# Optimization experiments

Hardware: AMD Instinct MI355X
Metric: run time of the kernel (lower is better)

Reference implementation:

```python
import jax, jax.numpy as jnp
import numpy as np

N_NODES = 50000
N_EDGES = 800000
D_IN = 128
D_HID = 128
BN_EPS = 1e-5


def _sage_mean(h, src, dst, w_self, w_neigh, b):
    # DGL SAGEConv('mean'): out = h @ W_self + mean_{neighbors}(h_src) @ W_neigh + bias
    msg = h[src]                                               # [E, D] gather
    ssum = jax.ops.segment_sum(msg, dst, num_segments=N_NODES)  # [N, D]
    deg = jax.ops.segment_sum(jnp.ones((src.shape[0],), h.dtype), dst,
                              num_segments=N_NODES)            # [N]
    mean = ssum / jnp.maximum(deg, 1.0)[:, None]
    return h @ w_self + mean @ w_neigh + b


def _bn_relu(h, gamma, beta):
    # BatchNorm1d with batch statistics (training-mode math), then ReLU.
    m = jnp.mean(h, axis=0)
    v = jnp.mean(jnp.square(h - m), axis=0)  # biased variance, as torch uses for normalization
    hn = (h - m) * jax.lax.rsqrt(v + BN_EPS) * gamma + beta
    return jax.nn.relu(hn)


def setup_inputs() -> dict:
    key = jax.random.key(0)
    ks = jax.random.split(key, 16)
    x = jax.random.normal(ks[0], (N_NODES, D_IN), dtype=jnp.float32)
    src = jax.random.randint(ks[1], (N_EDGES,), 0, N_NODES, dtype=jnp.int32)
    dst = jax.random.randint(ks[2], (N_EDGES,), 0, N_NODES, dtype=jnp.int32)
    s0 = 1.0 / np.sqrt(D_IN)
    s1 = 1.0 / np.sqrt(D_HID)
    inp = {
        'x': x, 'src': src, 'dst': dst,
        'W_self0': jax.random.uniform(ks[3], (D_IN, D_HID), jnp.float32, -s0, s0),
        'W_neigh0': jax.random.uniform(ks[4], (D_IN, D_HID), jnp.float32, -s0, s0),
        'b0': jnp.zeros((D_HID,), jnp.float32),
        'W_self1': jax.random.uniform(ks[5], (D_HID, D_HID), jnp.float32, -s1, s1),
        'W_neigh1': jax.random.uniform(ks[6], (D_HID, D_HID), jnp.float32, -s1, s1),
        'b1': jnp.zeros((D_HID,), jnp.float32),
        'W_self2': jax.random.uniform(ks[7], (D_HID, D_HID), jnp.float32, -s1, s1),
        'W_neigh2': jax.random.uniform(ks[8], (D_HID, D_HID), jnp.float32, -s1, s1),
        'b2': jnp.zeros((D_HID,), jnp.float32),
        'gamma0': jnp.ones((D_HID,), jnp.float32),
        'beta0': jnp.zeros((D_HID,), jnp.float32),
        'gamma1': jnp.ones((D_HID,), jnp.float32),
        'beta1': jnp.zeros((D_HID,), jnp.float32),
    }
    return inp


def reference(x, src, dst,
              W_self0, W_neigh0, b0,
              W_self1, W_neigh1, b1,
              W_self2, W_neigh2, b2,
              gamma0, beta0, gamma1, beta1):
    h = _sage_mean(x, src, dst, W_self0, W_neigh0, b0)
    h = _bn_relu(h, gamma0, beta0)  # dropout is identity in eval mode
    h = _sage_mean(h, src, dst, W_self1, W_neigh1, b1)
    h = _bn_relu(h, gamma1, beta1)
    h = _sage_mean(h, src, dst, W_self2, W_neigh2, b2)
    return h
```

## Files before the change

kernel.cpp:

```cpp
#include <hip/hip_runtime.h>

#define N_NODES 50000
#define N_EDGES 800000
#define D 128
#define BN_EPS 1e-5f

#define NBUCK 391
#define BSHIFT 7
#define S1_BLOCKS 256
#define EPB 3125
#define CVT_BLOCKS 6250
#define PACK_BLOCKS 384
#define NREP 8

typedef __attribute__((ext_vector_type(8))) short bf16x8;
typedef __attribute__((ext_vector_type(4))) float f32x4;

__device__ inline unsigned short f2bf(float f) {
    unsigned int u = __float_as_uint(f);
    u = (u + 0x7FFF + ((u >> 16) & 1)) >> 16;
    return (unsigned short)u;
}

__device__ inline float bf2f(unsigned short b) {
    return __uint_as_float(((unsigned)b) << 16);
}

__device__ __forceinline__ void acc_plain(float* a, uint4 v) {
    unsigned w[4] = {v.x, v.y, v.z, v.w};
#pragma unroll
    for (int p = 0; p < 4; p++) {
        a[2 * p]     += __uint_as_float(w[p] << 16);
        a[2 * p + 1] += __uint_as_float(w[p] & 0xffff0000u);
    }
}

__device__ __forceinline__ void acc_bn(float* a, uint4 v, const float* sc, const float* sh) {
    unsigned w[4] = {v.x, v.y, v.z, v.w};
#pragma unroll
    for (int p = 0; p < 4; p++) {
        float lo = __uint_as_float(w[p] << 16);
        float hi = __uint_as_float(w[p] & 0xffff0000u);
        a[2 * p]     += fmaxf(lo * sc[2 * p]     + sh[2 * p],     0.f);
        a[2 * p + 1] += fmaxf(hi * sc[2 * p + 1] + sh[2 * p + 1], 0.f);
    }
}


__global__ void fused_prep(const float* __restrict__ x, unsigned short* __restrict__ x16,
                           const int* __restrict__ dst, int* __restrict__ hist,
                           const float* __restrict__ Ws0, const float* __restrict__ Wn0,
                           const float* __restrict__ Ws1, const float* __restrict__ Wn1,
                           const float* __restrict__ Ws2, const float* __restrict__ Wn2,
                           unsigned short* __restrict__ Wf, float* __restrict__ statsg) {
    __shared__ int lh[NBUCK];
    const int bid = blockIdx.x, t = threadIdx.x;

    if (bid < CVT_BLOCKS) {
        int idx = bid * 256 + t;
        float4 v = ((const float4*)x)[idx];
        ushort4 o;
        o.x = f2bf(v.x); o.y = f2bf(v.y); o.z = f2bf(v.z); o.w = f2bf(v.w);
        ((ushort4*)x16)[idx] = o;
    } else if (bid < CVT_BLOCKS + S1_BLOCKS) {
        int blk = bid - CVT_BLOCKS;
        for (int i = t; i < NBUCK; i += 256) lh[i] = 0;
        __syncthreads();
        int e0 = blk * EPB;
        for (int i = 0; i < 13; i++) {
            int k = t + i * 256;
            if (k < EPB) atomicAdd(&lh[dst[e0 + k] >> BSHIFT], 1);
        }
        __syncthreads();
        for (int i = t; i < NBUCK; i += 256) hist[blk * NBUCK + i] = lh[i];
    } else {
        if (bid == CVT_BLOCKS + S1_BLOCKS) {
            for (int i = t; i < 2 * NREP * 256; i += 256) statsg[i] = 0.f;
        }
        int idx = (bid - (CVT_BLOCKS + S1_BLOCKS)) * 256 + t;
        if (idx < 3 * 32768) {
            int layer = idx >> 15;
            int rem = idx & 32767;
            int kt = rem >> 12;
            int nt = (rem >> 9) & 7;
            int lane = (rem >> 3) & 63;
            int j = rem & 7;
            int k = kt * 32 + (lane >> 4) * 8 + j;
            int n = nt * 16 + (lane & 15);
            const float* Wsrc;
            if (layer == 0) Wsrc = (k < 128) ? Ws0 : Wn0;
            else if (layer == 1) Wsrc = (k < 128) ? Ws1 : Wn1;
            else Wsrc = (k < 128) ? Ws2 : Wn2;
            Wf[idx] = f2bf(Wsrc[(k & 127) * D + n]);
        }
    }
}


__global__ void s2a(int* __restrict__ hist, int* __restrict__ bucketTotal) {
    __shared__ int s[S1_BLOCKS];
    int b = blockIdx.x, t = threadIdx.x;
    int v = hist[t * NBUCK + b];
    s[t] = v;
    __syncthreads();
    for (int off = 1; off < S1_BLOCKS; off <<= 1) {
        int x = (t >= off) ? s[t - off] : 0;
        __syncthreads();
        s[t] += x;
        __syncthreads();
    }
    hist[t * NBUCK + b] = s[t] - v;
    if (t == S1_BLOCKS - 1) bucketTotal[b] = s[t];
}


__global__ void s3_scatter(const int* __restrict__ src, const int* __restrict__ dst,
                           const int* __restrict__ hist, const int* __restrict__ bucketTotal,
                           int* __restrict__ bucketStart, unsigned int* __restrict__ rec) {
    __shared__ int sc[512];
    __shared__ int base[NBUCK];
    int blk = blockIdx.x, t = threadIdx.x;
    int i1 = t + 256;
    int v0 = (t < NBUCK) ? bucketTotal[t] : 0;
    int v1 = (i1 < NBUCK) ? bucketTotal[i1] : 0;
    sc[t] = v0; sc[i1] = v1;
    __syncthreads();
    for (int off = 1; off < 512; off <<= 1) {
        int x0 = (t >= off) ? sc[t - off] : 0;
        int x1 = (i1 >= off) ? sc[i1 - off] : 0;
        __syncthreads();
        sc[t] += x0; sc[i1] += x1;
        __syncthreads();
    }
    if (t < NBUCK)  base[t]  = (sc[t] - v0)  + hist[blk * NBUCK + t];
    if (i1 < NBUCK) base[i1] = (sc[i1] - v1) + hist[blk * NBUCK + i1];
    if (blk == 0) {
        if (t < NBUCK)  bucketStart[t]  = sc[t] - v0;
        if (i1 < NBUCK) bucketStart[i1] = sc[i1] - v1;
        if (t == 0) bucketStart[NBUCK] = N_EDGES;
    }
    __syncthreads();
    int e0 = blk * EPB;
    for (int i = 0; i < 13; i++) {
        int k = t + i * 256;
        if (k < EPB) {
            int e = e0 + k;
            int d = dst[e];
            int p = atomicAdd(&base[d >> BSHIFT], 1);
            rec[p] = ((unsigned)(d & 127) << 16) | (unsigned)src[e];
        }
    }
}


__global__ void s4_build(const unsigned int* __restrict__ rec, const int* __restrict__ bucketStart,
                         unsigned short* __restrict__ csr, int* __restrict__ degi,
                         int* __restrict__ offsets, float* __restrict__ inv_deg) {
    __shared__ int lh[128];
    __shared__ int ls[128];
    __shared__ int lcur[128];
    int b = blockIdx.x, t = threadIdx.x;
    int start = bucketStart[b], end = bucketStart[b + 1];

    if (t < 128) lh[t] = 0;
    __syncthreads();
    for (int e = start + t; e < end; e += 256)
        atomicAdd(&lh[rec[e] >> 16], 1);
    __syncthreads();

    int v = 0;
    if (t < 128) { v = lh[t]; ls[t] = v; }
    __syncthreads();
    for (int off = 1; off < 128; off <<= 1) {
        int x = 0;
        if (t < 128 && t >= off) x = ls[t - off];
        __syncthreads();
        if (t < 128) ls[t] += x;
        __syncthreads();
    }

    int node0 = b << BSHIFT;
    if (t < 128) {
        int excl = ls[t] - v;
        lcur[t] = start + excl;
        int node = node0 + t;
        if (node < N_NODES) {
            degi[node] = v;
            offsets[node] = start + excl;
            inv_deg[node] = 1.0f / (float)max(v, 1);
        }
    }
    __syncthreads();
    for (int e = start + t; e < end; e += 256) {
        unsigned r = rec[e];
        int p = atomicAdd(&lcur[r >> 16], 1);
        csr[p] = (unsigned short)(r & 0xFFFFu);
    }
}


#define GATHER(k) (*(const uint4*)(h16 + (size_t)csr[beg + (k)] * D + c * 8))

__global__ void aggregate16(const unsigned short* __restrict__ h16,
                            const unsigned short* __restrict__ csr, const int* __restrict__ offsets,
                            const int* __restrict__ degi, const float* __restrict__ inv_deg,
                            unsigned short* __restrict__ mean16,
                            const float* __restrict__ statsIn,
                            const float* __restrict__ gammaIn, const float* __restrict__ betaIn,
                            float* __restrict__ scshG) {
    int t = threadIdx.x;
    if (statsIn && blockIdx.x == 0 && t < 128) {
        const float invN = 1.0f / (float)N_NODES;
        float s = 0.f, q = 0.f;
#pragma unroll
        for (int r = 0; r < NREP; r++) {
            s += statsIn[r * 256 + t];
            q += statsIn[r * 256 + 128 + t];
        }
        float m = s * invN;
        float var = q * invN - m * m;
        float scv = rsqrtf(var + BN_EPS) * gammaIn[t];
        scshG[t] = scv;
        scshG[128 + t] = betaIn[t] - m * scv;
    }

    int node = blockIdx.x * 16 + (t >> 4);
    if (node >= N_NODES) return;
    int c = t & 15;
    int beg = offsets[node], n = degi[node];
    float a[8];
#pragma unroll
    for (int j = 0; j < 8; j++) a[j] = 0.f;

    if (statsIn) {
        const float invN = 1.0f / (float)N_NODES;
        float sc[8], sh[8];
#pragma unroll
        for (int j = 0; j < 8; j++) {
            int col = c * 8 + j;
            float s = 0.f, q = 0.f;
#pragma unroll
            for (int r = 0; r < NREP; r++) {
                s += statsIn[r * 256 + col];
                q += statsIn[r * 256 + 128 + col];
            }
            float m = s * invN;
            float var = q * invN - m * m;
            float scv = rsqrtf(var + BN_EPS) * gammaIn[col];
            sc[j] = scv;
            sh[j] = betaIn[col] - m * scv;
        }
        int i = 0;
        if (n >= 4) {
            uint4 v0 = GATHER(0), v1 = GATHER(1), v2 = GATHER(2), v3 = GATHER(3);
            for (i = 4; i + 3 < n; i += 4) {
                uint4 w0 = GATHER(i), w1 = GATHER(i + 1), w2 = GATHER(i + 2), w3 = GATHER(i + 3);
                acc_bn(a, v0, sc, sh); acc_bn(a, v1, sc, sh);
                acc_bn(a, v2, sc, sh); acc_bn(a, v3, sc, sh);
                v0 = w0; v1 = w1; v2 = w2; v3 = w3;
            }
            acc_bn(a, v0, sc, sh); acc_bn(a, v1, sc, sh);
            acc_bn(a, v2, sc, sh); acc_bn(a, v3, sc, sh);
        }
        for (; i < n; i++) { uint4 v = GATHER(i); acc_bn(a, v, sc, sh); }
    } else {
        int i = 0;
        if (n >= 4) {
            uint4 v0 = GATHER(0), v1 = GATHER(1), v2 = GATHER(2), v3 = GATHER(3);
            for (i = 4; i + 3 < n; i += 4) {
                uint4 w0 = GATHER(i), w1 = GATHER(i + 1), w2 = GATHER(i + 2), w3 = GATHER(i + 3);
                acc_plain(a, v0); acc_plain(a, v1); acc_plain(a, v2); acc_plain(a, v3);
                v0 = w0; v1 = w1; v2 = w2; v3 = w3;
            }
            acc_plain(a, v0); acc_plain(a, v1); acc_plain(a, v2); acc_plain(a, v3);
        }
        for (; i < n; i++) { uint4 v = GATHER(i); acc_plain(a, v); }
    }

    float w = inv_deg[node];
    uint4 o;
    o.x = ((unsigned)f2bf(a[1] * w) << 16) | f2bf(a[0] * w);
    o.y = ((unsigned)f2bf(a[3] * w) << 16) | f2bf(a[2] * w);
    o.z = ((unsigned)f2bf(a[5] * w) << 16) | f2bf(a[4] * w);
    o.w = ((unsigned)f2bf(a[7] * w) << 16) | f2bf(a[6] * w);
    *(uint4*)(mean16 + (size_t)node * D + c * 8) = o;
}


__global__ __launch_bounds__(256, 4) void sage_gemm(
    const unsigned short* __restrict__ h16, const unsigned short* __restrict__ mean16,
    const unsigned short* __restrict__ Wf, const float* __restrict__ bias,
    unsigned short* __restrict__ out16, float* __restrict__ outf,
    float* __restrict__ statsOut, const float* __restrict__ scshG) {
    __shared__ unsigned short sWf[16384];
    __shared__ float sstat[256];
    const int t = threadIdx.x;
    const int lane = t & 63;
    const int m = lane & 15;
    const int quad = lane >> 4;
    const int wrow0 = blockIdx.x * 64 + (t >> 6) * 16;

    int arow = wrow0 + m;
    if (arow >= N_NODES) arow = N_NODES - 1;

    bf16x8 afr[8];
#pragma unroll
    for (int kt = 0; kt < 4; kt++)
        afr[kt] = *(const bf16x8*)(h16 + (size_t)arow * D + kt * 32 + quad * 8);
#pragma unroll
    for (int kt = 0; kt < 4; kt++)
        afr[4 + kt] = *(const bf16x8*)(mean16 + (size_t)arow * D + kt * 32 + quad * 8);

    const uint4* W4 = (const uint4*)Wf;
    uint4* S4 = (uint4*)sWf;
#pragma unroll
    for (int i = 0; i < 8; i++) S4[i * 256 + t] = W4[i * 256 + t];
    if (statsOut) sstat[t] = 0.f;
    __syncthreads();

    if (scshG) {
#pragma unroll
        for (int kt = 0; kt < 4; kt++) {
            int c0 = kt * 32 + quad * 8;
            float4 sca = *(const float4*)(scshG + c0);
            float4 scb = *(const float4*)(scshG + c0 + 4);
            float4 sha = *(const float4*)(scshG + 128 + c0);
            float4 shb = *(const float4*)(scshG + 128 + c0 + 4);
            float scv[8] = {sca.x, sca.y, sca.z, sca.w, scb.x, scb.y, scb.z, scb.w};
            float shv[8] = {sha.x, sha.y, sha.z, sha.w, shb.x, shb.y, shb.z, shb.w};
#pragma unroll
            for (int j = 0; j < 8; j++) {
                float v = fmaxf(bf2f((unsigned short)afr[kt][j]) * scv[j] + shv[j], 0.f);
                afr[kt][j] = (short)f2bf(v);
            }
        }
    }

    f32x4 acc[8];
#pragma unroll
    for (int i = 0; i < 8; i++) acc[i] = (f32x4)(0.f);

#pragma unroll
    for (int kt = 0; kt < 4; kt++) {
#pragma unroll
        for (int nt = 0; nt < 8; nt++) {
            bf16x8 bf = *(const bf16x8*)(sWf + ((kt * 8 + nt) * 64 + lane) * 8);
            acc[nt] = __builtin_amdgcn_mfma_f32_16x16x32_bf16(afr[kt], bf, acc[nt], 0, 0, 0);
        }
    }

    __syncthreads();
#pragma unroll
    for (int i = 0; i < 8; i++) S4[i * 256 + t] = W4[2048 + i * 256 + t];
    __syncthreads();

#pragma unroll
    for (int kt = 4; kt < 8; kt++) {
#pragma unroll
        for (int nt = 0; nt < 8; nt++) {
            bf16x8 bf = *(const bf16x8*)(sWf + (((kt - 4) * 8 + nt) * 64 + lane) * 8);
            acc[nt] = __builtin_amdgcn_mfma_f32_16x16x32_bf16(afr[kt], bf, acc[nt], 0, 0, 0);
        }
    }

    const bool do16 = (out16 != nullptr);
#pragma unroll
    for (int nt = 0; nt < 8; nt++) {
        int cidx = nt * 16 + m;
        float bv = bias[cidx];
        float s = 0.f, q = 0.f;
#pragma unroll
        for (int reg = 0; reg < 4; reg++) {
            int r = wrow0 + quad * 4 + reg;
            float v = acc[nt][reg] + bv;
            if (r < N_NODES) {
                if (do16) out16[(size_t)r * D + cidx] = f2bf(v);
                else      outf[(size_t)r * D + cidx] = v;
                s += v; q += v * v;
            }
        }
        if (statsOut) {
            s += __shfl_xor(s, 16); s += __shfl_xor(s, 32);
            q += __shfl_xor(q, 16); q += __shfl_xor(q, 32);
            if (quad == 0) {
                atomicAdd(&sstat[cidx], s);
                atomicAdd(&sstat[128 + cidx], q);
            }
        }
    }
    if (statsOut) {
        __syncthreads();
        atomicAdd(&statsOut[(blockIdx.x & (NREP - 1)) * 256 + t], sstat[t]);
    }
}


extern "C" void kernel_launch(void* const* d_in, const int* in_sizes, int n_in,
                              void* d_out, int out_size, void* d_ws, size_t ws_size,
                              hipStream_t stream) {
    const float* x   = (const float*)d_in[0];
    const int* src   = (const int*)d_in[1];
    const int* dst   = (const int*)d_in[2];
    const float* Ws0 = (const float*)d_in[3];
    const float* Wn0 = (const float*)d_in[4];
    const float* b0  = (const float*)d_in[5];
    const float* Ws1 = (const float*)d_in[6];
    const float* Wn1 = (const float*)d_in[7];
    const float* b1  = (const float*)d_in[8];
    const float* Ws2 = (const float*)d_in[9];
    const float* Wn2 = (const float*)d_in[10];
    const float* b2  = (const float*)d_in[11];
    const float* g0  = (const float*)d_in[12];
    const float* be0 = (const float*)d_in[13];
    const float* g1  = (const float*)d_in[14];
    const float* be1 = (const float*)d_in[15];

    char* base = (char*)d_ws;
    size_t NND = (size_t)N_NODES * D;
    unsigned short* X16    = (unsigned short*)base;
    unsigned short* H16    = (unsigned short*)(base + NND * 2);
    unsigned short* mean16 = (unsigned short*)(base + 2 * NND * 2);
    char* p = base + 6 * NND;
    unsigned short* Wf = (unsigned short*)p;  p += 3 * 32768 * 2;
    int* hist          = (int*)p;             p += (size_t)S1_BLOCKS * NBUCK * 4;
    int* bucketTotal   = (int*)p;             p += 1568;
    int* bucketStart   = (int*)p;             p += 1600;
    unsigned int* rec  = (unsigned int*)p;    p += (size_t)N_EDGES * 4;
    unsigned short* csr = (unsigned short*)p; p += (size_t)N_EDGES * 2;
    int* degi    = (int*)p;                   p += N_NODES * 4;
    int* offsets = (int*)p;                   p += N_NODES * 4;
    float* inv_deg = (float*)p;               p += N_NODES * 4;
    float* stats   = (float*)p;               p += 2 * NREP * 256 * 4;
    float* scsh    = (float*)p;               p += 1024;
    float* stats0 = stats, *stats1 = stats + NREP * 256;

    fused_prep<<<CVT_BLOCKS + S1_BLOCKS + PACK_BLOCKS, 256, 0, stream>>>(
        x, X16, dst, hist, Ws0, Wn0, Ws1, Wn1, Ws2, Wn2, Wf, stats);
    s2a<<<NBUCK, 256, 0, stream>>>(hist, bucketTotal);
    s3_scatter<<<S1_BLOCKS, 256, 0, stream>>>(src, dst, hist, bucketTotal, bucketStart, rec);
    s4_build<<<NBUCK, 256, 0, stream>>>(rec, bucketStart, csr, degi, offsets, inv_deg);

    const int AGG_B = (N_NODES + 15) / 16;
    const int GEMM_B = (N_NODES + 63) / 64;

    aggregate16<<<AGG_B, 256, 0, stream>>>(X16, csr, offsets, degi, inv_deg, mean16,
                                           nullptr, nullptr, nullptr, nullptr);
    sage_gemm<<<GEMM_B, 256, 0, stream>>>(X16, mean16, Wf, b0, H16, nullptr,
                                          stats0, nullptr);

    aggregate16<<<AGG_B, 256, 0, stream>>>(H16, csr, offsets, degi, inv_deg, mean16,
                                           stats0, g0, be0, scsh);
    sage_gemm<<<GEMM_B, 256, 0, stream>>>(H16, mean16, Wf + 32768, b1, X16, nullptr,
                                          stats1, scsh);

    aggregate16<<<AGG_B, 256, 0, stream>>>(X16, csr, offsets, degi, inv_deg, mean16,
                                           stats1, g1, be1, scsh);
    sage_gemm<<<GEMM_B, 256, 0, stream>>>(X16, mean16, Wf + 65536, b2, nullptr,
                                          (float*)d_out, nullptr, scsh);
}
```

Before: 311.2 us.

## Sort CSR neighbors by source slice and apply BN-ReLU in separate pass

The CSR build now buckets each node's neighbors by the high bits of the source index, so gathers within a node run in roughly ascending source order. This aims for better cache locality during aggregation. BatchNorm+ReLU is no longer applied per edge inside aggregation and again in the GEMM prologue; a standalone elementwise kernel normalizes the hidden activations in place once. The stats replica count is also doubled to reduce atomic contention. The separate BN pass adds an extra read and write of the activation tensor and two more launches.

```diff
diff --git a/kernel.cpp b/kernel.cpp
--- a/kernel.cpp
+++ b/kernel.cpp
@@ -11,7 +11,10 @@
 #define EPB 3125
 #define CVT_BLOCKS 6250
 #define PACK_BLOCKS 384
-#define NREP 8
+#define NREP 16
+#define NSLICE 8
+#define SSHIFT 13
+#define BN_BLOCKS 512
 
 typedef __attribute__((ext_vector_type(8))) short bf16x8;
 typedef __attribute__((ext_vector_type(4))) float f32x4;
@@ -32,17 +35,6 @@
     for (int p = 0; p < 4; p++) {
         a[2 * p]     += __uint_as_float(w[p] << 16);
         a[2 * p + 1] += __uint_as_float(w[p] & 0xffff0000u);
-    }
-}
-
-__device__ __forceinline__ void acc_bn(float* a, uint4 v, const float* sc, const float* sh) {
-    unsigned w[4] = {v.x, v.y, v.z, v.w};
-#pragma unroll
-    for (int p = 0; p < 4; p++) {
-        float lo = __uint_as_float(w[p] << 16);
-        float hi = __uint_as_float(w[p] & 0xffff0000u);
-        a[2 * p]     += fmaxf(lo * sc[2 * p]     + sh[2 * p],     0.f);
-        a[2 * p + 1] += fmaxf(hi * sc[2 * p + 1] + sh[2 * p + 1], 0.f);
     }
 }
 
@@ -156,45 +148,101 @@
 __global__ void s4_build(const unsigned int* __restrict__ rec, const int* __restrict__ bucketStart,
                          unsigned short* __restrict__ csr, int* __restrict__ degi,
                          int* __restrict__ offsets, float* __restrict__ inv_deg) {
-    __shared__ int lh[128];
-    __shared__ int ls[128];
-    __shared__ int lcur[128];
+    __shared__ int cnt[128 * NSLICE];
+    __shared__ int exc[128 * NSLICE];
+    __shared__ int lcur[128 * NSLICE];
+    __shared__ int ls[256];
     int b = blockIdx.x, t = threadIdx.x;
     int start = bucketStart[b], end = bucketStart[b + 1];
 
-    if (t < 128) lh[t] = 0;
-    __syncthreads();
-    for (int e = start + t; e < end; e += 256)
-        atomicAdd(&lh[rec[e] >> 16], 1);
-    __syncthreads();
-
-    int v = 0;
-    if (t < 128) { v = lh[t]; ls[t] = v; }
-    __syncthreads();
-    for (int off = 1; off < 128; off <<= 1) {
-        int x = 0;
-        if (t < 128 && t >= off) x = ls[t - off];
-        __syncthreads();
-        if (t < 128) ls[t] += x;
-        __syncthreads();
-    }
-
-    int node0 = b << BSHIFT;
+    for (int i = t; i < 128 * NSLICE; i += 256) cnt[i] = 0;
+    __syncthreads();
+    for (int e = start + t; e < end; e += 256) {
+        unsigned r = rec[e];
+        int key = ((r >> 16) << 3) | ((r & 0xFFFFu) >> SSHIFT);
+        atomicAdd(&cnt[key], 1);
+    }
+    __syncthreads();
+
+    int c0 = cnt[4 * t], c1 = cnt[4 * t + 1], c2 = cnt[4 * t + 2], c3 = cnt[4 * t + 3];
+    int sum4 = c0 + c1 + c2 + c3;
+    ls[t] = sum4;
+    __syncthreads();
+    for (int off = 1; off < 256; off <<= 1) {
+        int x = (t >= off) ? ls[t - off] : 0;
+        __syncthreads();
+        ls[t] += x;
+        __syncthreads();
+    }
+    int base = ls[t] - sum4;
+    exc[4 * t]     = base;
+    exc[4 * t + 1] = base + c0;
+    exc[4 * t + 2] = base + c0 + c1;
+    exc[4 * t + 3] = base + c0 + c1 + c2;
+    lcur[4 * t]     = start + base;
+    lcur[4 * t + 1] = start + base + c0;
+    lcur[4 * t + 2] = start + base + c0 + c1;
+    lcur[4 * t + 3] = start + base + c0 + c1 + c2;
+    __syncthreads();
+
     if (t < 128) {
-        int excl = ls[t] - v;
-        lcur[t] = start + excl;
-        int node = node0 + t;
+        int node = (b << BSHIFT) + t;
+        int e0 = exc[8 * t];
+        int e1 = (t == 127) ? (end - start) : exc[8 * t + 8];
+        int v = e1 - e0;
         if (node < N_NODES) {
             degi[node] = v;
-            offsets[node] = start + excl;
+            offsets[node] = start + e0;
             inv_deg[node] = 1.0f / (float)max(v, 1);
         }
     }
     __syncthreads();
     for (int e = start + t; e < end; e += 256) {
         unsigned r = rec[e];
-        int p = atomicAdd(&lcur[r >> 16], 1);
+        int key = ((r >> 16) << 3) | ((r & 0xFFFFu) >> SSHIFT);
+        int p = atomicAdd(&lcur[key], 1);
         csr[p] = (unsigned short)(r & 0xFFFFu);
+    }
+}
+
+
+__global__ void bn_relu_apply(unsigned short* __restrict__ h,
+                              const float* __restrict__ stats,
+                              const float* __restrict__ gamma, const float* __restrict__ beta) {
+    __shared__ float sc[128], sh[128];
+    int t = threadIdx.x;
+    if (t < 128) {
+        const float invN = 1.0f / (float)N_NODES;
+        float s = 0.f, q = 0.f;
+#pragma unroll
+        for (int r = 0; r < NREP; r++) {
+            s += stats[r * 256 + t];
+            q += stats[r * 256 + 128 + t];
+        }
+        float m = s * invN;
+        float var = q * invN - m * m;
+        float scv = rsqrtf(var + BN_EPS) * gamma[t];
+        sc[t] = scv;
+        sh[t] = beta[t] - m * scv;
+    }
+    __syncthreads();
+    const int total = N_NODES * D / 8;
+    for (int idx = blockIdx.x * 256 + t; idx < total; idx += BN_BLOCKS * 256) {
+        uint4 v = ((const uint4*)h)[idx];
+        int col0 = (idx & 15) * 8;
+        unsigned w[4] = {v.x, v.y, v.z, v.w};
+        unsigned ow[4];
+#pragma unroll
+        for (int p = 0; p < 4; p++) {
+            float lo = __uint_as_float(w[p] << 16);
+            float hi = __uint_as_float(w[p] & 0xffff0000u);
+            float rlo = fmaxf(lo * sc[col0 + 2 * p]     + sh[col0 + 2 * p],     0.f);
+            float rhi = fmaxf(hi * sc[col0 + 2 * p + 1] + sh[col0 + 2 * p + 1], 0.f);
+            ow[p] = ((unsigned)f2bf(rhi) << 16) | f2bf(rlo);
+        }
+        uint4 o;
+        o.x = ow[0]; o.y = ow[1]; o.z = ow[2]; o.w = ow[3];
+        ((uint4*)h)[idx] = o;
     }
 }
 
@@ -204,26 +252,8 @@
 __global__ void aggregate16(const unsigned short* __restrict__ h16,
                             const unsigned short* __restrict__ csr, const int* __restrict__ offsets,
                             const int* __restrict__ degi, const float* __restrict__ inv_deg,
-                            unsigned short* __restrict__ mean16,
-                            const float* __restrict__ statsIn,
-                            const float* __restrict__ gammaIn, const float* __restrict__ betaIn,
-                            float* __restrict__ scshG) {
+                            unsigned short* __restrict__ mean16) {
     int t = threadIdx.x;
-    if (statsIn && blockIdx.x == 0 && t < 128) {
-        const float invN = 1.0f / (float)N_NODES;
-        float s = 0.f, q = 0.f;
-#pragma unroll
-        for (int r = 0; r < NREP; r++) {
-            s += statsIn[r * 256 + t];
-            q += statsIn[r * 256 + 128 + t];
-        }
-        float m = s * invN;
-        float var = q * invN - m * m;
-        float scv = rsqrtf(var + BN_EPS) * gammaIn[t];
-        scshG[t] = scv;
-        scshG[128 + t] = betaIn[t] - m * scv;
-    }
-
     int node = blockIdx.x * 16 + (t >> 4);
     if (node >= N_NODES) return;
     int c = t & 15;
@@ -232,50 +262,17 @@
 #pragma unroll
     for (int j = 0; j < 8; j++) a[j] = 0.f;
 
-    if (statsIn) {
-        const float invN = 1.0f / (float)N_NODES;
-        float sc[8], sh[8];
-#pragma unroll
-        for (int j = 0; j < 8; j++) {
-            int col = c * 8 + j;
-            float s = 0.f, q = 0.f;
-#pragma unroll
-            for (int r = 0; r < NREP; r++) {
-                s += statsIn[r * 256 + col];
-                q += statsIn[r * 256 + 128 + col];
-            }
-            float m = s * invN;
-            float var = q * invN - m * m;
-            float scv = rsqrtf(var + BN_EPS) * gammaIn[col];
-            sc[j] = scv;
-            sh[j] = betaIn[col] - m * scv;
-        }
-        int i = 0;
-        if (n >= 4) {
-            uint4 v0 = GATHER(0), v1 = GATHER(1), v2 = GATHER(2), v3 = GATHER(3);
-            for (i = 4; i + 3 < n; i += 4) {
-                uint4 w0 = GATHER(i), w1 = GATHER(i + 1), w2 = GATHER(i + 2), w3 = GATHER(i + 3);
-                acc_bn(a, v0, sc, sh); acc_bn(a, v1, sc, sh);
-                acc_bn(a, v2, sc, sh); acc_bn(a, v3, sc, sh);
-                v0 = w0; v1 = w1; v2 = w2; v3 = w3;
-            }
-            acc_bn(a, v0, sc, sh); acc_bn(a, v1, sc, sh);
-            acc_bn(a, v2, sc, sh); acc_bn(a, v3, sc, sh);
-        }
-        for (; i < n; i++) { uint4 v = GATHER(i); acc_bn(a, v, sc, sh); }
-    } else {
-        int i = 0;
-        if (n >= 4) {
-            uint4 v0 = GATHER(0), v1 = GATHER(1), v2 = GATHER(2), v3 = GATHER(3);
-            for (i = 4; i + 3 < n; i += 4) {
-                uint4 w0 = GATHER(i), w1 = GATHER(i + 1), w2 = GATHER(i + 2), w3 = GATHER(i + 3);
-                acc_plain(a, v0); acc_plain(a, v1); acc_plain(a, v2); acc_plain(a, v3);
-                v0 = w0; v1 = w1; v2 = w2; v3 = w3;
-            }
+    int i = 0;
+    if (n >= 4) {
+        uint4 v0 = GATHER(0), v1 = GATHER(1), v2 = GATHER(2), v3 = GATHER(3);
+        for (i = 4; i + 3 < n; i += 4) {
+            uint4 w0 = GATHER(i), w1 = GATHER(i + 1), w2 = GATHER(i + 2), w3 = GATHER(i + 3);
             acc_plain(a, v0); acc_plain(a, v1); acc_plain(a, v2); acc_plain(a, v3);
-        }
-        for (; i < n; i++) { uint4 v = GATHER(i); acc_plain(a, v); }
-    }
+            v0 = w0; v1 = w1; v2 = w2; v3 = w3;
+        }
+        acc_plain(a, v0); acc_plain(a, v1); acc_plain(a, v2); acc_plain(a, v3);
+    }
+    for (; i < n; i++) { uint4 v = GATHER(i); acc_plain(a, v); }
 
     float w = inv_deg[node];
     uint4 o;
@@ -291,7 +288,7 @@
     const unsigned short* __restrict__ h16, const unsigned short* __restrict__ mean16,
     const unsigned short* __restrict__ Wf, const float* __restrict__ bias,
     unsigned short* __restrict__ out16, float* __restrict__ outf,
-    float* __restrict__ statsOut, const float* __restrict__ scshG) {
+    float* __restrict__ statsOut) {
     __shared__ unsigned short sWf[16384];
     __shared__ float sstat[256];
     const int t = threadIdx.x;
@@ -317,24 +314,6 @@
     for (int i = 0; i < 8; i++) S4[i * 256 + t] = W4[i * 256 + t];
     if (statsOut) sstat[t] = 0.f;
     __syncthreads();
-
-    if (scshG) {
-#pragma unroll
-        for (int kt = 0; kt < 4; kt++) {
-            int c0 = kt * 32 + quad * 8;
-            float4 sca = *(const float4*)(scshG + c0);
-            float4 scb = *(const float4*)(scshG + c0 + 4);
-            float4 sha = *(const float4*)(scshG + 128 + c0);
-            float4 shb = *(const float4*)(scshG + 128 + c0 + 4);
-            float scv[8] = {sca.x, sca.y, sca.z, sca.w, scb.x, scb.y, scb.z, scb.w};
-            float shv[8] = {sha.x, sha.y, sha.z, sha.w, shb.x, shb.y, shb.z, shb.w};
-#pragma unroll
-            for (int j = 0; j < 8; j++) {
-                float v = fmaxf(bf2f((unsigned short)afr[kt][j]) * scv[j] + shv[j], 0.f);
-                afr[kt][j] = (short)f2bf(v);
-            }
-        }
-    }
 
     f32x4 acc[8];
 #pragma unroll
@@ -431,7 +410,6 @@
     int* offsets = (int*)p;                   p += N_NODES * 4;
     float* inv_deg = (float*)p;               p += N_NODES * 4;
     float* stats   = (float*)p;               p += 2 * NREP * 256 * 4;
-    float* scsh    = (float*)p;               p += 1024;
     float* stats0 = stats, *stats1 = stats + NREP * 256;
 
     fused_prep<<<CVT_BLOCKS + S1_BLOCKS + PACK_BLOCKS, 256, 0, stream>>>(
@@ -443,18 +421,15 @@
     const int AGG_B = (N_NODES + 15) / 16;
     const int GEMM_B = (N_NODES + 63) / 64;
 
-    aggregate16<<<AGG_B, 256, 0, stream>>>(X16, csr, offsets, degi, inv_deg, mean16,
-                                           nullptr, nullptr, nullptr, nullptr);
-    sage_gemm<<<GEMM_B, 256, 0, stream>>>(X16, mean16, Wf, b0, H16, nullptr,
-                                          stats0, nullptr);
-
-    aggregate16<<<AGG_B, 256, 0, stream>>>(H16, csr, offsets, degi, inv_deg, mean16,
-                                           stats0, g0, be0, scsh);
-    sage_gemm<<<GEMM_B, 256, 0, stream>>>(H16, mean16, Wf + 32768, b1, X16, nullptr,
-                                          stats1, scsh);
-
-    aggregate16<<<AGG_B, 256, 0, stream>>>(X16, csr, offsets, degi, inv_deg, mean16,
-                                           stats1, g1, be1, scsh);
+    aggregate16<<<AGG_B, 256, 0, stream>>>(X16, csr, offsets, degi, inv_deg, mean16);
+    sage_gemm<<<GEMM_B, 256, 0, stream>>>(X16, mean16, Wf, b0, H16, nullptr, stats0);
+
+    bn_relu_apply<<<BN_BLOCKS, 256, 0, stream>>>(H16, stats0, g0, be0);
+    aggregate16<<<AGG_B, 256, 0, stream>>>(H16, csr, offsets, degi, inv_deg, mean16);
+    sage_gemm<<<GEMM_B, 256, 0, stream>>>(H16, mean16, Wf + 32768, b1, X16, nullptr, stats1);
+
+    bn_relu_apply<<<BN_BLOCKS, 256, 0, stream>>>(X16, stats1, g1, be1);
+    aggregate16<<<AGG_B, 256, 0, stream>>>(X16, csr, offsets, degi, inv_deg, mean16);
     sage_gemm<<<GEMM_B, 256, 0, stream>>>(X16, mean16, Wf + 65536, b2, nullptr,
-                                          (float*)d_out, nullptr, scsh);
-}
+                                          (float*)d_out, nullptr);
+}
```

Result: faster. 279.6 us (-10.1%).
